# Performance work log

Hardware: AMD Instinct MI355X
Metric: run time of the kernel (lower is better)

## Reference

```python
import jax, jax.numpy as jnp
import numpy as np

B, C, T = 8, 256, 16000
N_HALF = 32  # d_state // 2 complex modes (S4D stores conjugate pairs)
EPS = 1e-8


def setup_inputs() -> dict:
    key = jax.random.key(0)
    ks = jax.random.split(key, 8)
    x = jax.random.normal(ks[0], (B, C, T), jnp.float32)
    # ChannelwiseLayerNorm params
    gamma = jnp.ones((C,), jnp.float32)
    beta = jnp.zeros((C,), jnp.float32)
    # PReLU per-channel slope (torch default init 0.25)
    prelu_w = jnp.full((C,), 0.25, jnp.float32)
    # S4D kernel params (standard S4D init)
    log_dt = (jax.random.uniform(ks[1], (C,), jnp.float32)
              * (np.log(0.1) - np.log(0.001)) + np.log(0.001)).astype(jnp.float32)
    log_A_real = jnp.log(0.5 * jnp.ones((C, N_HALF), jnp.float32))
    A_imag = jnp.broadcast_to(np.pi * jnp.arange(N_HALF, dtype=jnp.float32), (C, N_HALF))
    C_re = jax.random.normal(ks[2], (C, N_HALF), jnp.float32) * (0.5 ** 0.5)
    C_im = jax.random.normal(ks[3], (C, N_HALF), jnp.float32) * (0.5 ** 0.5)
    D = jax.random.normal(ks[4], (C,), jnp.float32)
    # output 1x1 conv (C -> 2C) followed by GLU over channel dim
    W_out = jax.random.normal(ks[5], (2 * C, C), jnp.float32) * (1.0 / np.sqrt(C))
    b_out = jnp.zeros((2 * C,), jnp.float32)
    return dict(x=x, gamma=gamma, beta=beta, prelu_w=prelu_w, log_dt=log_dt,
                log_A_real=log_A_real, A_imag=A_imag, C_re=C_re, C_im=C_im,
                D=D, W_out=W_out, b_out=b_out)


def reference(x, gamma, beta, prelu_w, log_dt, log_A_real, A_imag, C_re, C_im, D, W_out, b_out):
    # --- channel-wise LayerNorm over C (per timestep), x: [B, C, T] ---
    mean = jnp.mean(x, axis=1, keepdims=True)
    var = jnp.mean((x - mean) ** 2, axis=1, keepdims=True)
    y = (x - mean) * jax.lax.rsqrt(var + EPS)
    y = y * gamma[None, :, None] + beta[None, :, None]
    # --- PReLU (per-channel slope) ---
    y = jnp.where(y >= 0, y, prelu_w[None, :, None] * y)
    # --- S4D convolution kernel via Vandermonde (ZOH discretization) ---
    L = x.shape[-1]
    dt = jnp.exp(log_dt)[:, None]                      # [C, 1]
    A = -jnp.exp(log_A_real) + 1j * A_imag             # [C, N]
    dtA = dt * A                                       # [C, N]
    Cc = (C_re + 1j * C_im) * (jnp.exp(dtA) - 1.0) / A  # [C, N]
    vand = jnp.exp(dtA[:, :, None] * jnp.arange(L))    # [C, N, L]
    k = 2.0 * jnp.real(jnp.einsum('hn,hnl->hl', Cc, vand))  # [C, L]
    # --- FFT-based causal convolution ---
    n = 2 * L
    y_f = jnp.fft.rfft(y, n=n)                         # [B, C, n/2+1]
    k_f = jnp.fft.rfft(k, n=n)                         # [C, n/2+1]
    s = jnp.fft.irfft(y_f * k_f[None], n=n)[..., :L]   # [B, C, T]
    s = s + y * D[None, :, None]                       # skip connection
    # --- GELU + 1x1 conv + GLU over channels ---
    s = jax.nn.gelu(s, approximate=False)
    z = jnp.einsum('bct,oc->bot', s, W_out) + b_out[None, :, None]  # [B, 2C, T]
    out = z[:, :C] * jax.nn.sigmoid(z[:, C:])
    # --- residual ---
    return x + out
```

## Files before the change

kernel.cpp:

```cpp
#include <hip/hip_runtime.h>
#include <cstdint>
#include <cstddef>

constexpr int cB = 8, cC = 256, cT = 16000, cN = 32;
constexpr int cP = 125;
constexpr float cEPS = 1e-8f;

typedef __bf16 bf16;
typedef __bf16 bf16x4 __attribute__((ext_vector_type(4)));
typedef __bf16 bf16x8 __attribute__((ext_vector_type(8)));
typedef float floatx4 __attribute__((ext_vector_type(4)));

constexpr size_t kMean = 0;
constexpr size_t kRstd = kMean + (size_t)cB * cT * 4;
constexpr size_t kWlr  = kRstd + (size_t)cB * cT * 4;
constexpr size_t kWli  = kWlr + (size_t)cC * cN * 4;
constexpr size_t kWb   = kWli + (size_t)cC * cN * 4;
constexpr size_t kLt   = kWb  + (size_t)512 * 256 * 2;
constexpr size_t kEt   = kLt  + (size_t)cC * 128 * 128 * 2;
constexpr size_t kVt   = kEt  + (size_t)cC * 64 * 128 * 2;
constexpr size_t kU    = kVt  + (size_t)cC * 128 * 64 * 2;

__device__ __forceinline__ float fast_sigmoid(float z) {
  return __builtin_amdgcn_rcpf(1.f + __builtin_amdgcn_exp2f(-z * 1.4426950408889634f));
}

__global__ void prepW_kernel(const float* __restrict__ W_out, bf16* __restrict__ Wb) {
  int idx = blockIdx.x * 256 + threadIdx.x;
  if (idx < 512 * 256) Wb[idx] = (bf16)W_out[idx];
}

__global__ void prep2_kernel(const float* __restrict__ log_dt,
                             const float* __restrict__ log_A_real,
                             const float* __restrict__ A_imag,
                             const float* __restrict__ C_re,
                             const float* __restrict__ C_im,
                             float* __restrict__ wlr, float* __restrict__ wli,
                             bf16* __restrict__ Lt, bf16* __restrict__ Et,
                             bf16* __restrict__ Vt) {
  int c = blockIdx.x;
  int j = threadIdx.x;
  __shared__ float kv[128];
  float dt = expf(log_dt[c]);
  float kj = 0.f;
  for (int n = 0; n < cN; ++n) {
    int idx = c * cN + n;
    float Ar = -expf(log_A_real[idx]);
    float Ai = A_imag[idx];
    float ar = dt * Ar, ai = dt * Ai;
    float mg = expf(ar), cw, sw;
    sincosf(ai, &sw, &cw);
    float wre = mg * cw, wim = mg * sw;
    float den = Ar * Ar + Ai * Ai;
    float emr = wre - 1.f, emi = wim;
    float qr = (emr * Ar + emi * Ai) / den;
    float qi = (emi * Ar - emr * Ai) / den;
    float cre = C_re[idx], cim = C_im[idx];
    float c2r = 2.f * (cre * qr - cim * qi);
    float c2i = 2.f * (cre * qi + cim * qr);
    float mj = expf((float)j * ar), cj, sj;
    sincosf((float)j * ai, &sj, &cj);
    float wjr = mj * cj, wji = mj * sj;
    kj += c2r * wjr - c2i * wji;
    float w1r = wjr * wre - wji * wim;
    float w1i = wjr * wim + wji * wre;
    Vt[(size_t)c * 8192 + j * 64 + 2 * n]     = (bf16)(c2r * w1r - c2i * w1i);
    Vt[(size_t)c * 8192 + j * 64 + 2 * n + 1] = (bf16)(-(c2r * w1i + c2i * w1r));
    float mr = expf((float)(127 - j) * ar), cr2, sr2;
    sincosf((float)(127 - j) * ai, &sr2, &cr2);
    Et[(size_t)c * 8192 + (2 * n) * 128 + j]     = (bf16)(mr * cr2);
    Et[(size_t)c * 8192 + (2 * n + 1) * 128 + j] = (bf16)(mr * sr2);
  }
  kv[j] = kj;
  if (j < cN) {
    int idx = c * cN + j;
    float Ar = -expf(log_A_real[idx]);
    float ai = dt * A_imag[idx], ar = dt * Ar;
    float m = expf(128.f * ar), cc, ss;
    sincosf(128.f * ai, &ss, &cc);
    wlr[idx] = m * cc;
    wli[idx] = m * ss;
  }
  __syncthreads();
  bf16* LtC = Lt + (size_t)c * 16384;
  for (int e = j; e < 4096; e += 128) {
    int t4 = e * 4;
    int row = t4 >> 7, col = t4 & 127;
    bf16x4 v;
#pragma unroll
    for (int q = 0; q < 4; ++q) {
      int ii = col + q;
      v[q] = (ii <= row) ? (bf16)kv[row - ii] : (bf16)0.f;
    }
    *(bf16x4*)(LtC + row * 128 + col) = v;
  }
}

__global__ __launch_bounds__(512)
void stats_kernel(const float* __restrict__ x,
                  float* __restrict__ meanp, float* __restrict__ rstdp) {
  __shared__ float r1[8][64], r2[8][64];
  int g0 = blockIdx.x * 64;
  int b = g0 / cT;
  int t0 = g0 - b * cT;
  int ts = threadIdx.x & 63, cq = threadIdx.x >> 6;
  const float* xp = x + ((size_t)b * cC + cq * 32) * cT + t0 + ts;
  float s1 = 0.f, s2 = 0.f;
#pragma unroll 8
  for (int c = 0; c < 32; ++c) {
    float v = xp[(size_t)c * cT];
    s1 += v;
    s2 = fmaf(v, v, s2);
  }
  r1[cq][ts] = s1; r2[cq][ts] = s2;
  __syncthreads();
  if (threadIdx.x < 64) {
    float a1 = 0.f, a2 = 0.f;
#pragma unroll
    for (int q = 0; q < 8; ++q) { a1 += r1[q][threadIdx.x]; a2 += r2[q][threadIdx.x]; }
    float mean = a1 * (1.0f / cC);
    float var = fmaf(a2, 1.0f / cC, -mean * mean);
    int g = g0 + threadIdx.x;
    meanp[g] = mean;
    rstdp[g] = rsqrtf(var + cEPS);
  }
}

__global__ __launch_bounds__(256, 2)
void scanM_kernel(const float* __restrict__ x, const float* __restrict__ meanp,
                  const float* __restrict__ rstdp, const float* __restrict__ gam,
                  const float* __restrict__ bet, const float* __restrict__ prw,
                  const float* __restrict__ Dp,
                  const float* __restrict__ wlr, const float* __restrict__ wli,
                  const bf16* __restrict__ Lt, const bf16* __restrict__ Et,
                  const bf16* __restrict__ Vt, bf16* __restrict__ U) {
  __shared__ __align__(16) bf16 Y[128 * 136];
  __shared__ __align__(16) bf16 H[128 * 136];
  __shared__ float Sseg[8][32][2];

  int blk = blockIdx.x;
  int b = blk & 7, c = blk >> 3;
  int tid = threadIdx.x;
  int lane = tid & 63, w = tid >> 6, quad = lane >> 4, mh = lane & 15;
  float gamma = gam[c], beta = bet[c], pw = prw[c], Dc = Dp[c];

  const float4* x4 = (const float4*)(x + (size_t)(b * cC + c) * cT);
  const float4* m4 = (const float4*)(meanp + (size_t)b * cT);
  const float4* r4 = (const float4*)(rstdp + (size_t)b * cT);
#pragma unroll
  for (int it = 0; it < 16; ++it) {
    int i4 = tid + it * 256;
    if (i4 < 4000) {
      float4 xv = x4[i4], mv = m4[i4], rv = r4[i4];
      int t = i4 * 4, p = t >> 7, j = t & 127;
      float ys[4];
      ys[0] = fmaf((xv.x - mv.x) * rv.x, gamma, beta);
      ys[1] = fmaf((xv.y - mv.y) * rv.y, gamma, beta);
      ys[2] = fmaf((xv.z - mv.z) * rv.z, gamma, beta);
      ys[3] = fmaf((xv.w - mv.w) * rv.w, gamma, beta);
      bf16x4 yv;
#pragma unroll
      for (int q = 0; q < 4; ++q) {
        float y = ys[q];
        yv[q] = (bf16)(y >= 0.f ? y : y * pw);
      }
      *(bf16x4*)&Y[p * 136 + j] = yv;
    }
  }
  for (int e = tid; e < 3 * 136; e += 256) Y[125 * 136 + e] = (bf16)0.f;
  __syncthreads();

  const bf16* EtC = Et + (size_t)c * 8192;
  floatx4 hacc[8];
#pragma unroll
  for (int mi = 0; mi < 8; ++mi) hacc[mi] = (floatx4){0.f, 0.f, 0.f, 0.f};
#pragma unroll
  for (int kk = 0; kk < 4; ++kk) {
    bf16x8 bfrag = *(const bf16x8*)(EtC + (w * 16 + mh) * 128 + kk * 32 + quad * 8);
#pragma unroll
    for (int mi = 0; mi < 8; ++mi) {
      bf16x8 af = *(bf16x8*)&Y[(mi * 16 + mh) * 136 + kk * 32 + quad * 8];
      hacc[mi] = __builtin_amdgcn_mfma_f32_16x16x32_bf16(af, bfrag, hacc[mi], 0, 0, 0);
    }
  }
#pragma unroll
  for (int mi = 0; mi < 8; ++mi) {
#pragma unroll
    for (int r = 0; r < 4; ++r) {
      int p = mi * 16 + quad * 4 + r;
      int comp = w * 16 + mh;
      float v = hacc[mi][r];
      bf16 hi = (bf16)v;
      bf16 lo = (bf16)(v - (float)hi);
      H[p * 136 + comp] = hi;
      H[p * 136 + 64 + comp] = lo;
    }
  }
  __syncthreads();

  {
    int n = tid & 31, sg = tid >> 5;
    int p0 = sg * 16;
    int p1 = (p0 + 16 < cP) ? p0 + 16 : cP;
    float wr = wlr[c * cN + n], wi = wli[c * cN + n];
    float hR = 0.f, hI = 0.f;
    for (int p = p0; p < p1; ++p) {
      float sr = (float)H[p * 136 + 2 * n] + (float)H[p * 136 + 64 + 2 * n];
      float si = (float)H[p * 136 + 2 * n + 1] + (float)H[p * 136 + 64 + 2 * n + 1];
      float t1 = fmaf(wr, hR, fmaf(-wi, hI, sr));
      hI = fmaf(wr, hI, fmaf(wi, hR, si));
      hR = t1;
    }
    Sseg[sg][n][0] = hR; Sseg[sg][n][1] = hI;
    __syncthreads();
    if (tid < 32) {
      float ar = wr, ai = wi;
      for (int q = 0; q < 4; ++q) {
        float nr = ar * ar - ai * ai;
        ai = 2.f * ar * ai; ar = nr;
      }
      float HR = 0.f, HI = 0.f;
      for (int s2 = 0; s2 < 8; ++s2) {
        float fr = Sseg[s2][n][0], fi = Sseg[s2][n][1];
        Sseg[s2][n][0] = HR; Sseg[s2][n][1] = HI;
        float t1 = fmaf(ar, HR, fmaf(-ai, HI, fr));
        HI = fmaf(ar, HI, fmaf(ai, HR, fi));
        HR = t1;
      }
    }
    __syncthreads();
    hR = Sseg[sg][n][0]; hI = Sseg[sg][n][1];
    for (int p = p0; p < p1; ++p) {
      float sr = (float)H[p * 136 + 2 * n] + (float)H[p * 136 + 64 + 2 * n];
      float si = (float)H[p * 136 + 2 * n + 1] + (float)H[p * 136 + 64 + 2 * n + 1];
      bf16 hiR = (bf16)hR; bf16 loR = (bf16)(hR - (float)hiR);
      bf16 hiI = (bf16)hI; bf16 loI = (bf16)(hI - (float)hiI);
      H[p * 136 + 2 * n] = hiR;      H[p * 136 + 2 * n + 1] = hiI;
      H[p * 136 + 64 + 2 * n] = loR; H[p * 136 + 64 + 2 * n + 1] = loI;
      float t1 = fmaf(wr, hR, fmaf(-wi, hI, sr));
      hI = fmaf(wr, hI, fmaf(wi, hR, si));
      hR = t1;
    }
  }
  __syncthreads();

  const bf16* LtC = Lt + (size_t)c * 16384;
  const bf16* VtC = Vt + (size_t)c * 8192;
  floatx4 acc[8][2];
#pragma unroll
  for (int mi = 0; mi < 8; ++mi) {
    acc[mi][0] = (floatx4){0.f, 0.f, 0.f, 0.f};
    acc[mi][1] = (floatx4){0.f, 0.f, 0.f, 0.f};
  }
#pragma unroll
  for (int kk = 0; kk < 4; ++kk) {
    bf16x8 b0 = *(const bf16x8*)(LtC + ((2 * w) * 16 + mh) * 128 + kk * 32 + quad * 8);
    bf16x8 b1 = *(const bf16x8*)(LtC + ((2 * w + 1) * 16 + mh) * 128 + kk * 32 + quad * 8);
#pragma unroll
    for (int mi = 0; mi < 8; ++mi) {
      bf16x8 af = *(bf16x8*)&Y[(mi * 16 + mh) * 136 + kk * 32 + quad * 8];
      acc[mi][0] = __builtin_amdgcn_mfma_f32_16x16x32_bf16(af, b0, acc[mi][0], 0, 0, 0);
      acc[mi][1] = __builtin_amdgcn_mfma_f32_16x16x32_bf16(af, b1, acc[mi][1], 0, 0, 0);
    }
  }
#pragma unroll
  for (int kk = 0; kk < 2; ++kk) {
    bf16x8 v0 = *(const bf16x8*)(VtC + ((2 * w) * 16 + mh) * 64 + kk * 32 + quad * 8);
    bf16x8 v1 = *(const bf16x8*)(VtC + ((2 * w + 1) * 16 + mh) * 64 + kk * 32 + quad * 8);
#pragma unroll
    for (int mi = 0; mi < 8; ++mi) {
      bf16x8 ah = *(bf16x8*)&H[(mi * 16 + mh) * 136 + kk * 32 + quad * 8];
      bf16x8 al = *(bf16x8*)&H[(mi * 16 + mh) * 136 + 64 + kk * 32 + quad * 8];
      acc[mi][0] = __builtin_amdgcn_mfma_f32_16x16x32_bf16(ah, v0, acc[mi][0], 0, 0, 0);
      acc[mi][1] = __builtin_amdgcn_mfma_f32_16x16x32_bf16(ah, v1, acc[mi][1], 0, 0, 0);
      acc[mi][0] = __builtin_amdgcn_mfma_f32_16x16x32_bf16(al, v0, acc[mi][0], 0, 0, 0);
      acc[mi][1] = __builtin_amdgcn_mfma_f32_16x16x32_bf16(al, v1, acc[mi][1], 0, 0, 0);
    }
  }
  bf16 ub[8][2][4];
#pragma unroll
  for (int mi = 0; mi < 8; ++mi)
#pragma unroll
    for (int jj = 0; jj < 2; ++jj)
#pragma unroll
      for (int r = 0; r < 4; ++r) {
        int p = mi * 16 + quad * 4 + r;
        int j = (2 * w + jj) * 16 + mh;
        float y = (float)Y[p * 136 + j];
        float sv = fmaf(Dc, y, acc[mi][jj][r]);
        float s3 = sv * sv * sv;
        float zz = 0.7978845608028654f * fmaf(0.044715f, s3, sv);
        float e = __builtin_amdgcn_exp2f(zz * 2.8853900817779268f);
        float th = 1.f - 2.f * __builtin_amdgcn_rcpf(e + 1.f);
        float g = 0.5f * sv * (1.f + th);
        ub[mi][jj][r] = (bf16)g;
      }
  __syncthreads();
#pragma unroll
  for (int mi = 0; mi < 8; ++mi)
#pragma unroll
    for (int jj = 0; jj < 2; ++jj)
#pragma unroll
      for (int r = 0; r < 4; ++r) {
        int p = mi * 16 + quad * 4 + r;
        int j = (2 * w + jj) * 16 + mh;
        Y[p * 136 + j] = ub[mi][jj][r];
      }
  __syncthreads();
  bf16* Uc = U + (size_t)(b * cC + c) * cT;
#pragma unroll
  for (int it = 0; it < 16; ++it) {
    int i4 = tid + it * 256;
    if (i4 < 4000) {
      int t = i4 * 4, p = t >> 7, j = t & 127;
      *(bf16x4*)(Uc + t) = *(bf16x4*)&Y[p * 136 + j];
    }
  }
}

__global__ __launch_bounds__(512, 4)
void gemm2_kernel(const bf16* __restrict__ U, const bf16* __restrict__ Wb,
                  const float* __restrict__ b_out, const float* __restrict__ x,
                  float* __restrict__ out) {
  __shared__ __align__(16) bf16 Ut[64 * 264];
  int bx = blockIdx.x;
  int tb = bx % 250, b = bx / 250;
  int t0 = tb * 64;
  int tid = threadIdx.x, lane = tid & 63, w = tid >> 6, quad = lane >> 4, mh = lane & 15;
  {
    int c = tid & 255, th = tid >> 8;
    const bf16* src = U + (size_t)(b * cC + c) * cT + t0 + th * 32;
#pragma unroll
    for (int g = 0; g < 4; ++g) {
      bf16x8 v = *(const bf16x8*)(src + g * 8);
#pragma unroll
      for (int k = 0; k < 8; ++k) Ut[(th * 32 + g * 8 + k) * 264 + c] = v[k];
    }
  }
  __syncthreads();
  floatx4 a1[2][4], a2[2][4];
#pragma unroll
  for (int oj = 0; oj < 2; ++oj)
#pragma unroll
    for (int tt = 0; tt < 4; ++tt) {
      a1[oj][tt] = (floatx4){0.f, 0.f, 0.f, 0.f};
      a2[oj][tt] = (floatx4){0.f, 0.f, 0.f, 0.f};
    }
#pragma unroll
  for (int kk = 0; kk < 8; ++kk) {
    int ko = kk * 32 + quad * 8;
    bf16x8 wf1[2], wf2[2];
#pragma unroll
    for (int oj = 0; oj < 2; ++oj) {
      int o = w * 32 + oj * 16 + mh;
      wf1[oj] = *(const bf16x8*)(Wb + (size_t)o * 256 + ko);
      wf2[oj] = *(const bf16x8*)(Wb + (size_t)(o + 256) * 256 + ko);
    }
#pragma unroll
    for (int tt = 0; tt < 4; ++tt) {
      bf16x8 uf = *(bf16x8*)&Ut[(tt * 16 + mh) * 264 + ko];
#pragma unroll
      for (int oj = 0; oj < 2; ++oj) {
        a1[oj][tt] = __builtin_amdgcn_mfma_f32_16x16x32_bf16(wf1[oj], uf, a1[oj][tt], 0, 0, 0);
        a2[oj][tt] = __builtin_amdgcn_mfma_f32_16x16x32_bf16(wf2[oj], uf, a2[oj][tt], 0, 0, 0);
      }
    }
  }
#pragma unroll
  for (int oj = 0; oj < 2; ++oj)
#pragma unroll
    for (int tt = 0; tt < 4; ++tt)
#pragma unroll
      for (int r = 0; r < 4; ++r) {
        int o = w * 32 + oj * 16 + quad * 4 + r;
        int t = t0 + tt * 16 + mh;
        float z1 = a1[oj][tt][r] + b_out[o];
        float z2 = a2[oj][tt][r] + b_out[o + 256];
        float sg = fast_sigmoid(z2);
        size_t idx = (size_t)(b * cC + o) * cT + t;
        out[idx] = x[idx] + z1 * sg;
      }
}

extern "C" void kernel_launch(void* const* d_in, const int* in_sizes, int n_in,
                              void* d_out, int out_size, void* d_ws, size_t ws_size,
                              hipStream_t stream) {
  const float* x          = (const float*)d_in[0];
  const float* gamma      = (const float*)d_in[1];
  const float* beta       = (const float*)d_in[2];
  const float* prelu_w    = (const float*)d_in[3];
  const float* log_dt     = (const float*)d_in[4];
  const float* log_A_real = (const float*)d_in[5];
  const float* A_imag     = (const float*)d_in[6];
  const float* C_re       = (const float*)d_in[7];
  const float* C_im       = (const float*)d_in[8];
  const float* Dp         = (const float*)d_in[9];
  const float* W_out      = (const float*)d_in[10];
  const float* b_out      = (const float*)d_in[11];
  float* out = (float*)d_out;
  char* ws = (char*)d_ws;

  float* meanp = (float*)(ws + kMean);
  float* rstdp = (float*)(ws + kRstd);
  float* wlr   = (float*)(ws + kWlr);
  float* wli   = (float*)(ws + kWli);
  bf16*  Wb    = (bf16*)(ws + kWb);
  bf16*  Lt    = (bf16*)(ws + kLt);
  bf16*  Et    = (bf16*)(ws + kEt);
  bf16*  Vt    = (bf16*)(ws + kVt);
  bf16*  U     = (bf16*)(ws + kU);

  prepW_kernel<<<512, 256, 0, stream>>>(W_out, Wb);
  prep2_kernel<<<256, 128, 0, stream>>>(log_dt, log_A_real, A_imag, C_re, C_im,
                                        wlr, wli, Lt, Et, Vt);
  stats_kernel<<<(cB * cT) / 64, 512, 0, stream>>>(x, meanp, rstdp);
  scanM_kernel<<<cB * cC, 256, 0, stream>>>(x, meanp, rstdp, gamma, beta, prelu_w,
                                            Dp, wlr, wli, Lt, Et, Vt, U);
  gemm2_kernel<<<cB * (cT / 64), 512, 0, stream>>>(U, Wb, b_out, x, out);
}
```

Measured before the change: 467.8 us.

## Widen scan kernel to 512 threads, remap blocks, vectorize stats loads

The scan/convolution kernel moves from 256 to 512 threads per block. The MFMA work is split across 8 waves, with each wave owning one 16-column tile instead of two, and the H projection is split by column group and row half. Block indices are remapped so that consecutive blocks share a batch instead of a channel, which changes the L2 locality of the x/mean/rstd reads. The stats kernel reads float2 and handles 128 timesteps per block. Half the threads sit idle during the serial scan phase, and the higher occupancy target may cause register pressure.

```diff
diff --git a/kernel.cpp b/kernel.cpp
--- a/kernel.cpp
+++ b/kernel.cpp
@@ -99,25 +99,26 @@
 __global__ __launch_bounds__(512)
 void stats_kernel(const float* __restrict__ x,
                   float* __restrict__ meanp, float* __restrict__ rstdp) {
-  __shared__ float r1[8][64], r2[8][64];
-  int g0 = blockIdx.x * 64;
+  __shared__ float S1[8][128], S2[8][128];
+  int g0 = blockIdx.x * 128;
   int b = g0 / cT;
   int t0 = g0 - b * cT;
-  int ts = threadIdx.x & 63, cq = threadIdx.x >> 6;
-  const float* xp = x + ((size_t)b * cC + cq * 32) * cT + t0 + ts;
-  float s1 = 0.f, s2 = 0.f;
+  int tp = threadIdx.x & 63, cq = threadIdx.x >> 6;
+  const float2* xp = (const float2*)(x + ((size_t)b * cC + cq * 32) * cT + t0) + tp;
+  float s1x = 0.f, s1y = 0.f, s2x = 0.f, s2y = 0.f;
 #pragma unroll 8
-  for (int c = 0; c < 32; ++c) {
-    float v = xp[(size_t)c * cT];
-    s1 += v;
-    s2 = fmaf(v, v, s2);
-  }
-  r1[cq][ts] = s1; r2[cq][ts] = s2;
-  __syncthreads();
-  if (threadIdx.x < 64) {
+  for (int cc = 0; cc < 32; ++cc) {
+    float2 v = xp[(size_t)cc * (cT / 2)];
+    s1x += v.x; s2x = fmaf(v.x, v.x, s2x);
+    s1y += v.y; s2y = fmaf(v.y, v.y, s2y);
+  }
+  S1[cq][2 * tp] = s1x; S1[cq][2 * tp + 1] = s1y;
+  S2[cq][2 * tp] = s2x; S2[cq][2 * tp + 1] = s2y;
+  __syncthreads();
+  if (threadIdx.x < 128) {
     float a1 = 0.f, a2 = 0.f;
 #pragma unroll
-    for (int q = 0; q < 8; ++q) { a1 += r1[q][threadIdx.x]; a2 += r2[q][threadIdx.x]; }
+    for (int q = 0; q < 8; ++q) { a1 += S1[q][threadIdx.x]; a2 += S2[q][threadIdx.x]; }
     float mean = a1 * (1.0f / cC);
     float var = fmaf(a2, 1.0f / cC, -mean * mean);
     int g = g0 + threadIdx.x;
@@ -126,7 +127,7 @@
   }
 }
 
-__global__ __launch_bounds__(256, 2)
+__global__ __launch_bounds__(512, 4)
 void scanM_kernel(const float* __restrict__ x, const float* __restrict__ meanp,
                   const float* __restrict__ rstdp, const float* __restrict__ gam,
                   const float* __restrict__ bet, const float* __restrict__ prw,
@@ -139,17 +140,18 @@
   __shared__ float Sseg[8][32][2];
 
   int blk = blockIdx.x;
-  int b = blk & 7, c = blk >> 3;
+  int logical = (blk & 7) * 256 + (blk >> 3);
+  int b = logical & 7, c = logical >> 3;
   int tid = threadIdx.x;
-  int lane = tid & 63, w = tid >> 6, quad = lane >> 4, mh = lane & 15;
+  int lane = tid & 63, w8 = tid >> 6, quad = lane >> 4, mh = lane & 15;
   float gamma = gam[c], beta = bet[c], pw = prw[c], Dc = Dp[c];
 
   const float4* x4 = (const float4*)(x + (size_t)(b * cC + c) * cT);
   const float4* m4 = (const float4*)(meanp + (size_t)b * cT);
   const float4* r4 = (const float4*)(rstdp + (size_t)b * cT);
 #pragma unroll
-  for (int it = 0; it < 16; ++it) {
-    int i4 = tid + it * 256;
+  for (int it = 0; it < 8; ++it) {
+    int i4 = tid + it * 512;
     if (i4 < 4000) {
       float4 xv = x4[i4], mv = m4[i4], rv = r4[i4];
       int t = i4 * 4, p = t >> 7, j = t & 127;
@@ -167,28 +169,29 @@
       *(bf16x4*)&Y[p * 136 + j] = yv;
     }
   }
-  for (int e = tid; e < 3 * 136; e += 256) Y[125 * 136 + e] = (bf16)0.f;
+  for (int e = tid; e < 3 * 136; e += 512) Y[125 * 136 + e] = (bf16)0.f;
   __syncthreads();
 
   const bf16* EtC = Et + (size_t)c * 8192;
-  floatx4 hacc[8];
-#pragma unroll
-  for (int mi = 0; mi < 8; ++mi) hacc[mi] = (floatx4){0.f, 0.f, 0.f, 0.f};
+  int cgrp = (w8 & 3) * 16, mbase = (w8 >> 2) * 4;
+  floatx4 hacc[4];
+#pragma unroll
+  for (int mi = 0; mi < 4; ++mi) hacc[mi] = (floatx4){0.f, 0.f, 0.f, 0.f};
 #pragma unroll
   for (int kk = 0; kk < 4; ++kk) {
-    bf16x8 bfrag = *(const bf16x8*)(EtC + (w * 16 + mh) * 128 + kk * 32 + quad * 8);
-#pragma unroll
-    for (int mi = 0; mi < 8; ++mi) {
-      bf16x8 af = *(bf16x8*)&Y[(mi * 16 + mh) * 136 + kk * 32 + quad * 8];
+    bf16x8 bfrag = *(const bf16x8*)(EtC + (cgrp + mh) * 128 + kk * 32 + quad * 8);
+#pragma unroll
+    for (int mi = 0; mi < 4; ++mi) {
+      bf16x8 af = *(bf16x8*)&Y[((mbase + mi) * 16 + mh) * 136 + kk * 32 + quad * 8];
       hacc[mi] = __builtin_amdgcn_mfma_f32_16x16x32_bf16(af, bfrag, hacc[mi], 0, 0, 0);
     }
   }
 #pragma unroll
-  for (int mi = 0; mi < 8; ++mi) {
+  for (int mi = 0; mi < 4; ++mi) {
 #pragma unroll
     for (int r = 0; r < 4; ++r) {
-      int p = mi * 16 + quad * 4 + r;
-      int comp = w * 16 + mh;
+      int p = (mbase + mi) * 16 + quad * 4 + r;
+      int comp = cgrp + mh;
       float v = hacc[mi][r];
       bf16 hi = (bf16)v;
       bf16 lo = (bf16)(v - (float)hi);
@@ -199,19 +202,21 @@
   __syncthreads();
 
   {
-    int n = tid & 31, sg = tid >> 5;
+    int n = tid & 31, sg = (tid >> 5) & 7;
     int p0 = sg * 16;
     int p1 = (p0 + 16 < cP) ? p0 + 16 : cP;
     float wr = wlr[c * cN + n], wi = wli[c * cN + n];
     float hR = 0.f, hI = 0.f;
-    for (int p = p0; p < p1; ++p) {
-      float sr = (float)H[p * 136 + 2 * n] + (float)H[p * 136 + 64 + 2 * n];
-      float si = (float)H[p * 136 + 2 * n + 1] + (float)H[p * 136 + 64 + 2 * n + 1];
-      float t1 = fmaf(wr, hR, fmaf(-wi, hI, sr));
-      hI = fmaf(wr, hI, fmaf(wi, hR, si));
-      hR = t1;
-    }
-    Sseg[sg][n][0] = hR; Sseg[sg][n][1] = hI;
+    if (tid < 256) {
+      for (int p = p0; p < p1; ++p) {
+        float sr = (float)H[p * 136 + 2 * n] + (float)H[p * 136 + 64 + 2 * n];
+        float si = (float)H[p * 136 + 2 * n + 1] + (float)H[p * 136 + 64 + 2 * n + 1];
+        float t1 = fmaf(wr, hR, fmaf(-wi, hI, sr));
+        hI = fmaf(wr, hI, fmaf(wi, hR, si));
+        hR = t1;
+      }
+      Sseg[sg][n][0] = hR; Sseg[sg][n][1] = hI;
+    }
     __syncthreads();
     if (tid < 32) {
       float ar = wr, ai = wi;
@@ -229,88 +234,76 @@
       }
     }
     __syncthreads();
-    hR = Sseg[sg][n][0]; hI = Sseg[sg][n][1];
-    for (int p = p0; p < p1; ++p) {
-      float sr = (float)H[p * 136 + 2 * n] + (float)H[p * 136 + 64 + 2 * n];
-      float si = (float)H[p * 136 + 2 * n + 1] + (float)H[p * 136 + 64 + 2 * n + 1];
-      bf16 hiR = (bf16)hR; bf16 loR = (bf16)(hR - (float)hiR);
-      bf16 hiI = (bf16)hI; bf16 loI = (bf16)(hI - (float)hiI);
-      H[p * 136 + 2 * n] = hiR;      H[p * 136 + 2 * n + 1] = hiI;
-      H[p * 136 + 64 + 2 * n] = loR; H[p * 136 + 64 + 2 * n + 1] = loI;
-      float t1 = fmaf(wr, hR, fmaf(-wi, hI, sr));
-      hI = fmaf(wr, hI, fmaf(wi, hR, si));
-      hR = t1;
+    if (tid < 256) {
+      hR = Sseg[sg][n][0]; hI = Sseg[sg][n][1];
+      for (int p = p0; p < p1; ++p) {
+        float sr = (float)H[p * 136 + 2 * n] + (float)H[p * 136 + 64 + 2 * n];
+        float si = (float)H[p * 136 + 2 * n + 1] + (float)H[p * 136 + 64 + 2 * n + 1];
+        bf16 hiR = (bf16)hR; bf16 loR = (bf16)(hR - (float)hiR);
+        bf16 hiI = (bf16)hI; bf16 loI = (bf16)(hI - (float)hiI);
+        H[p * 136 + 2 * n] = hiR;      H[p * 136 + 2 * n + 1] = hiI;
+        H[p * 136 + 64 + 2 * n] = loR; H[p * 136 + 64 + 2 * n + 1] = loI;
+        float t1 = fmaf(wr, hR, fmaf(-wi, hI, sr));
+        hI = fmaf(wr, hI, fmaf(wi, hR, si));
+        hR = t1;
+      }
     }
   }
   __syncthreads();
 
   const bf16* LtC = Lt + (size_t)c * 16384;
   const bf16* VtC = Vt + (size_t)c * 8192;
-  floatx4 acc[8][2];
-#pragma unroll
-  for (int mi = 0; mi < 8; ++mi) {
-    acc[mi][0] = (floatx4){0.f, 0.f, 0.f, 0.f};
-    acc[mi][1] = (floatx4){0.f, 0.f, 0.f, 0.f};
-  }
+  floatx4 acc[8];
+#pragma unroll
+  for (int mi = 0; mi < 8; ++mi) acc[mi] = (floatx4){0.f, 0.f, 0.f, 0.f};
 #pragma unroll
   for (int kk = 0; kk < 4; ++kk) {
-    bf16x8 b0 = *(const bf16x8*)(LtC + ((2 * w) * 16 + mh) * 128 + kk * 32 + quad * 8);
-    bf16x8 b1 = *(const bf16x8*)(LtC + ((2 * w + 1) * 16 + mh) * 128 + kk * 32 + quad * 8);
+    bf16x8 b0 = *(const bf16x8*)(LtC + (w8 * 16 + mh) * 128 + kk * 32 + quad * 8);
 #pragma unroll
     for (int mi = 0; mi < 8; ++mi) {
       bf16x8 af = *(bf16x8*)&Y[(mi * 16 + mh) * 136 + kk * 32 + quad * 8];
-      acc[mi][0] = __builtin_amdgcn_mfma_f32_16x16x32_bf16(af, b0, acc[mi][0], 0, 0, 0);
-      acc[mi][1] = __builtin_amdgcn_mfma_f32_16x16x32_bf16(af, b1, acc[mi][1], 0, 0, 0);
+      acc[mi] = __builtin_amdgcn_mfma_f32_16x16x32_bf16(af, b0, acc[mi], 0, 0, 0);
     }
   }
 #pragma unroll
   for (int kk = 0; kk < 2; ++kk) {
-    bf16x8 v0 = *(const bf16x8*)(VtC + ((2 * w) * 16 + mh) * 64 + kk * 32 + quad * 8);
-    bf16x8 v1 = *(const bf16x8*)(VtC + ((2 * w + 1) * 16 + mh) * 64 + kk * 32 + quad * 8);
+    bf16x8 v0 = *(const bf16x8*)(VtC + (w8 * 16 + mh) * 64 + kk * 32 + quad * 8);
 #pragma unroll
     for (int mi = 0; mi < 8; ++mi) {
       bf16x8 ah = *(bf16x8*)&H[(mi * 16 + mh) * 136 + kk * 32 + quad * 8];
       bf16x8 al = *(bf16x8*)&H[(mi * 16 + mh) * 136 + 64 + kk * 32 + quad * 8];
-      acc[mi][0] = __builtin_amdgcn_mfma_f32_16x16x32_bf16(ah, v0, acc[mi][0], 0, 0, 0);
-      acc[mi][1] = __builtin_amdgcn_mfma_f32_16x16x32_bf16(ah, v1, acc[mi][1], 0, 0, 0);
-      acc[mi][0] = __builtin_amdgcn_mfma_f32_16x16x32_bf16(al, v0, acc[mi][0], 0, 0, 0);
-      acc[mi][1] = __builtin_amdgcn_mfma_f32_16x16x32_bf16(al, v1, acc[mi][1], 0, 0, 0);
-    }
-  }
-  bf16 ub[8][2][4];
+      acc[mi] = __builtin_amdgcn_mfma_f32_16x16x32_bf16(ah, v0, acc[mi], 0, 0, 0);
+      acc[mi] = __builtin_amdgcn_mfma_f32_16x16x32_bf16(al, v0, acc[mi], 0, 0, 0);
+    }
+  }
+  bf16 ub[8][4];
+  int jcol = w8 * 16 + mh;
 #pragma unroll
   for (int mi = 0; mi < 8; ++mi)
 #pragma unroll
-    for (int jj = 0; jj < 2; ++jj)
-#pragma unroll
-      for (int r = 0; r < 4; ++r) {
-        int p = mi * 16 + quad * 4 + r;
-        int j = (2 * w + jj) * 16 + mh;
-        float y = (float)Y[p * 136 + j];
-        float sv = fmaf(Dc, y, acc[mi][jj][r]);
-        float s3 = sv * sv * sv;
-        float zz = 0.7978845608028654f * fmaf(0.044715f, s3, sv);
-        float e = __builtin_amdgcn_exp2f(zz * 2.8853900817779268f);
-        float th = 1.f - 2.f * __builtin_amdgcn_rcpf(e + 1.f);
-        float g = 0.5f * sv * (1.f + th);
-        ub[mi][jj][r] = (bf16)g;
-      }
+    for (int r = 0; r < 4; ++r) {
+      int p = mi * 16 + quad * 4 + r;
+      float y = (float)Y[p * 136 + jcol];
+      float sv = fmaf(Dc, y, acc[mi][r]);
+      float s3 = sv * sv * sv;
+      float zz = 0.7978845608028654f * fmaf(0.044715f, s3, sv);
+      float e = __builtin_amdgcn_exp2f(zz * 2.8853900817779268f);
+      float th = 1.f - 2.f * __builtin_amdgcn_rcpf(e + 1.f);
+      ub[mi][r] = (bf16)(0.5f * sv * (1.f + th));
+    }
   __syncthreads();
 #pragma unroll
   for (int mi = 0; mi < 8; ++mi)
 #pragma unroll
-    for (int jj = 0; jj < 2; ++jj)
-#pragma unroll
-      for (int r = 0; r < 4; ++r) {
-        int p = mi * 16 + quad * 4 + r;
-        int j = (2 * w + jj) * 16 + mh;
-        Y[p * 136 + j] = ub[mi][jj][r];
-      }
+    for (int r = 0; r < 4; ++r) {
+      int p = mi * 16 + quad * 4 + r;
+      Y[p * 136 + jcol] = ub[mi][r];
+    }
   __syncthreads();
   bf16* Uc = U + (size_t)(b * cC + c) * cT;
 #pragma unroll
-  for (int it = 0; it < 16; ++it) {
-    int i4 = tid + it * 256;
+  for (int it = 0; it < 8; ++it) {
+    int i4 = tid + it * 512;
     if (i4 < 4000) {
       int t = i4 * 4, p = t >> 7, j = t & 127;
       *(bf16x4*)(Uc + t) = *(bf16x4*)&Y[p * 136 + j];
@@ -413,8 +406,8 @@
   prepW_kernel<<<512, 256, 0, stream>>>(W_out, Wb);
   prep2_kernel<<<256, 128, 0, stream>>>(log_dt, log_A_real, A_imag, C_re, C_im,
                                         wlr, wli, Lt, Et, Vt);
-  stats_kernel<<<(cB * cT) / 64, 512, 0, stream>>>(x, meanp, rstdp);
-  scanM_kernel<<<cB * cC, 256, 0, stream>>>(x, meanp, rstdp, gamma, beta, prelu_w,
+  stats_kernel<<<(cB * cT) / 128, 512, 0, stream>>>(x, meanp, rstdp);
+  scanM_kernel<<<cB * cC, 512, 0, stream>>>(x, meanp, rstdp, gamma, beta, prelu_w,
                                             Dp, wlr, wli, Lt, Et, Vt, U);
   gemm2_kernel<<<cB * (cT / 64), 512, 0, stream>>>(U, Wb, b_out, x, out);
 }
```

Result: no change. 458.7 us (-1.9%).
